# Optimization experiments

Hardware: AMD Instinct MI355X
Metric: run time of the kernel (lower is better)

## Reference

```python
import jax, jax.numpy as jnp
import numpy as np

N_NODES = 50000
N_EDGES = 800000
D = 128          # input_node_dim == output_node_dim (residual)
T = 3            # number of node types == number of edge types
NODE_IN = D + T * D  # node updater input dim = 512


def setup_inputs() -> dict:
    key = jax.random.key(0)
    ks = jax.random.split(key, 8)
    scale = 0.05
    return {
        "node_feature": jax.random.normal(ks[0], (N_NODES, D), jnp.float32),
        "W_e": jax.random.normal(ks[1], (T, D, D), jnp.float32) * scale,
        "b_e": jnp.zeros((T, D), jnp.float32),
        "W_n": jax.random.normal(ks[2], (T, D, NODE_IN), jnp.float32) * scale,
        "b_n": jnp.zeros((T, D), jnp.float32),
        "edge_src": jax.random.randint(ks[3], (N_EDGES,), 0, N_NODES, jnp.int32),
        "edge_dst": jax.random.randint(ks[4], (N_EDGES,), 0, N_NODES, jnp.int32),
        "edge_type": jax.random.randint(ks[5], (N_EDGES,), 0, T, jnp.int32),
        "node_type": jax.random.randint(ks[6], (N_NODES,), 0, T, jnp.int32),
    }


def reference(node_feature, W_e, b_e, W_n, b_n, edge_src, edge_dst, edge_type, node_type):
    N, Din = node_feature.shape
    n_types = W_e.shape[0]
    out_dim = W_e.shape[1]

    # message_function: per-edge-type MLP on source features, relu, zero elsewhere
    src = node_feature[edge_src]                      # [E, D] gather
    parts = [jax.nn.relu(node_feature)]               # reduce_function relu's node_feature
    for t in range(n_types):
        msg = jax.nn.relu(src @ W_e[t].T + b_e[t])    # [E, out]
        msg = jnp.where((edge_type == t)[:, None], msg, jnp.zeros((), msg.dtype))
        # mailbox sum over incoming edges per destination node
        parts.append(jax.ops.segment_sum(msg, edge_dst, num_segments=N))
    agg = jnp.concatenate(parts, axis=1)              # [N, D + T*out]

    # per-node-type updater MLP, dispatched by node_type
    updated = jnp.zeros((N, out_dim), node_feature.dtype)
    for t in range(n_types):
        o = agg @ W_n[t].T + b_n[t]                   # [N, out]
        updated = jnp.where((node_type == t)[:, None], o, updated)

    # use_residual = True
    return updated + node_feature
```

## Files before the change

kernel.cpp:

```cpp
#include <hip/hip_runtime.h>
#include <hip/hip_bf16.h>

#define NN 50000
#define NE 800000
#define DD 128
#define NT 3
#define AGGW 384
#define EM 64
#define EM2 128
#define LDK 136
#define CB 32
#define LDK2 520
#define NBITS 7
#define NBINS ((NN + 127) / 128)
#define EPB 2048
#define BINCAP 2560
#define NTILES_MAX (((NN + EM - 1) / EM) + NT)
#define NTILE_PAD (((NTILES_MAX + 7) / 8) * 8)
#define LHS 392

typedef __bf16 bf16x8 __attribute__((ext_vector_type(8)));
typedef float f32x4 __attribute__((ext_vector_type(4)));
typedef unsigned short u16x8 __attribute__((ext_vector_type(8)));
typedef unsigned int u32x4 __attribute__((ext_vector_type(4)));

__device__ __forceinline__ unsigned short f2b(float f) {
    __hip_bfloat16 h = __float2bfloat16(f);
    return __builtin_bit_cast(unsigned short, h);
}
__device__ __forceinline__ float b2f(unsigned int u16bits) {
    unsigned int x = u16bits << 16;
    return __builtin_bit_cast(float, x);
}

__global__ void k_prep(const float* __restrict__ nf, const float* __restrict__ We,
                       const float* __restrict__ Wn, unsigned short* __restrict__ nfb,
                       unsigned short* __restrict__ Web, unsigned short* __restrict__ Wnb,
                       int* __restrict__ bhist, int* __restrict__ cnts) {
    size_t i = (size_t)blockIdx.x * blockDim.x + threadIdx.x;
    if (i < NBINS) bhist[i] = 0;
    if (i >= NBINS && i < NBINS + 16) cnts[i - NBINS] = 0;
    const size_t n0 = (size_t)NN * DD / 8;
    const size_t n1 = (size_t)NT * DD * DD / 8;
    const size_t n2 = (size_t)NT * DD * 512 / 8;
    size_t total = n0 + n1 + n2;
    for (size_t p = i; p < total; p += (size_t)gridDim.x * blockDim.x) {
        const float* s; unsigned short* d; size_t off;
        if (p < n0)            { s = nf; d = nfb; off = p; }
        else if (p < n0 + n1)  { s = We; d = Web; off = p - n0; }
        else                   { s = Wn; d = Wnb; off = p - n0 - n1; }
        const float4* f4 = (const float4*)(s + off * 8);
        float4 x = f4[0], y = f4[1];
        u16x8 u = { f2b(x.x), f2b(x.y), f2b(x.z), f2b(x.w),
                    f2b(y.x), f2b(y.y), f2b(y.z), f2b(y.w) };
        *(u16x8*)(d + off * 8) = u;
    }
}

__global__ __launch_bounds__(256) void k_binhist(const int* __restrict__ edst,
        const int* __restrict__ ntp, int* __restrict__ bhist, int* __restrict__ cnts) {
    __shared__ int lh[NBINS];
    __shared__ int ln[3];
    int tid = threadIdx.x;
    for (int i = tid; i < NBINS; i += 256) lh[i] = 0;
    if (tid < 3) ln[tid] = 0;
    __syncthreads();
    int i0 = blockIdx.x * blockDim.x + tid;
    int stride = gridDim.x * blockDim.x;
    for (int p = i0; p < NE; p += stride) atomicAdd(&lh[edst[p] >> NBITS], 1);
    for (int p = i0; p < NN; p += stride) atomicAdd(&ln[ntp[p]], 1);
    __syncthreads();
    for (int i = tid; i < NBINS; i += 256) if (lh[i]) atomicAdd(&bhist[i], lh[i]);
    if (tid < 3) atomicAdd(&cnts[6 + tid], ln[tid]);
}

__global__ __launch_bounds__(512) void k_binscan(const int* __restrict__ bhist,
        int* __restrict__ binptr, int* __restrict__ bincur, int* __restrict__ rowptr) {
    __shared__ int sa[NBINS], sb[NBINS];
    int tid = threadIdx.x;
    if (tid < NBINS) sa[tid] = bhist[tid];
    __syncthreads();
    int flip = 0;
    for (int off = 1; off < NBINS; off <<= 1) {
        int* src = flip ? sb : sa;
        int* dst = flip ? sa : sb;
        if (tid < NBINS) dst[tid] = src[tid] + ((tid >= off) ? src[tid - off] : 0);
        __syncthreads();
        flip ^= 1;
    }
    int* inc = flip ? sb : sa;
    if (tid < NBINS) {
        int excl = (tid == 0) ? 0 : inc[tid - 1];
        binptr[tid] = excl;
        bincur[tid] = excl;
    }
    if (tid == 0) { binptr[NBINS] = NE; rowptr[NN] = NE; }
}

__global__ __launch_bounds__(512) void k_mid(
        const unsigned short* __restrict__ nfb, const unsigned short* __restrict__ Web,
        const float* __restrict__ be, unsigned short* __restrict__ M,
        const int* __restrict__ esrc, const int* __restrict__ edst,
        const int* __restrict__ et, const int* __restrict__ ntp,
        int* __restrict__ bincur, int* __restrict__ cnts,
        int* __restrict__ pe, int* __restrict__ sn, int* __restrict__ rnk) {
    const int NEB = (NE + EPB - 1) / EPB;
    const int NCH2 = (NN + 511) / 512;
    const int TILES = (NN + EM2 - 1) / EM2;
    __shared__ unsigned short Wsm[DD][LDK];
    int tid = threadIdx.x, b = blockIdx.x;

    if (b < NEB) {
        int* lh = (int*)&Wsm[0][0];
        int* lr = lh + 8 * LHS;
        int* gb = lr + 8 * LHS;
        int wv = tid >> 6, ln = tid & 63;
        for (int i = tid; i < 8 * LHS; i += 512) { lh[i] = 0; lr[i] = 0; }
        __syncthreads();
        int ew0 = b * EPB + wv * 256;
#pragma unroll
        for (int i = 0; i < 256; i += 64) {
            int e = ew0 + i + ln;
            if (e < NE) atomicAdd(&lh[wv * LHS + (edst[e] >> NBITS)], 1);
        }
        __syncthreads();
        for (int i = tid; i < NBINS; i += 512) {
            int s = 0;
#pragma unroll
            for (int w = 0; w < 8; ++w) { int t = lh[w * LHS + i]; lh[w * LHS + i] = s; s += t; }
            if (s) gb[i] = atomicAdd(&bincur[i], s);
        }
        __syncthreads();
#pragma unroll
        for (int i = 0; i < 256; i += 64) {
            int e = ew0 + i + ln;
            if (e < NE) {
                int d = edst[e];
                int t = et[e];
                int bin = d >> NBITS;
                int pos = gb[bin] + lh[wv * LHS + bin] + atomicAdd(&lr[wv * LHS + bin], 1);
                pe[pos] = (t * NN + esrc[e]) | ((d & 127) << 18) | (t << 25);
            }
        }
    } else if (b < NEB + NCH2) {
        int* lcnt = (int*)&Wsm[0][0];
        int* lbase = lcnt + 4;
        if (tid < 3) lcnt[tid] = 0;
        __syncthreads();
        int p = (b - NEB) * 512 + tid;
        int t = -1, rank = 0;
        if (p < NN) { t = ntp[p]; rank = atomicAdd(&lcnt[t], 1); }
        __syncthreads();
        if (tid < 3) lbase[tid] = atomicAdd(&cnts[9 + tid], lcnt[tid]);
        __syncthreads();
        if (p < NN) {
            int c0 = cnts[6], c1 = cnts[7];
            int off = (t == 0) ? 0 : (t == 1) ? c0 : c0 + c1;
            int pos = off + lbase[t] + rank;
            sn[pos] = p;
            rnk[p] = pos;
        }
    } else {
        int bb = b - NEB - NCH2;
        int t = bb / TILES, tile = bb % TILES;
        int base = tile * EM2;
        int m = min(EM2, NN - base);
        {
            int row = tid >> 2, c0 = (tid & 3) * 32;
            const u16x8* src = (const u16x8*)(Web + ((size_t)t * DD + row) * DD + c0);
#pragma unroll
            for (int v = 0; v < 4; ++v) *(u16x8*)&Wsm[row][c0 + v * 8] = src[v];
        }
        __syncthreads();

        int wave = tid >> 6, l = tid & 63, lr2 = l & 15, kg = l >> 4;
        int arow = min(base + wave * 16 + lr2, NN - 1);
        const u16x8* Arow = (const u16x8*)(nfb + (size_t)arow * DD);
        f32x4 acc[8];
#pragma unroll
        for (int n = 0; n < 8; n++) acc[n] = (f32x4){0.f, 0.f, 0.f, 0.f};
#pragma unroll
        for (int k0 = 0; k0 < DD; k0 += 32) {
            bf16x8 a = __builtin_bit_cast(bf16x8, Arow[(k0 >> 3) + kg]);
#pragma unroll
            for (int n = 0; n < 8; n++) {
                bf16x8 bbv = *(const bf16x8*)&Wsm[n * 16 + lr2][k0 + kg * 8];
                acc[n] = __builtin_amdgcn_mfma_f32_16x16x32_bf16(a, bbv, acc[n], 0, 0, 0);
            }
        }
        unsigned short* Mt = M + (size_t)t * NN * DD;
#pragma unroll
        for (int n = 0; n < 8; n++) {
            int col = n * 16 + lr2;
            float bias = be[t * DD + col];
#pragma unroll
            for (int r = 0; r < 4; r++) {
                int row = wave * 16 + kg * 4 + r;
                if (row < m) {
                    float v = acc[n][r] + bias;
                    Mt[(size_t)(base + row) * DD + col] = f2b(fmaxf(v, 0.f));
                }
            }
        }
    }
}

__global__ __launch_bounds__(256) void k_binsort(const int* __restrict__ binptr,
        int* __restrict__ pe, int* __restrict__ rowptr) {
    __shared__ int lcnt[128], lrk[128], lrp[128];
    __shared__ unsigned int sorted[BINCAP];
    int b = blockIdx.x, tid = threadIdx.x;
    int beg = binptr[b], end = binptr[b + 1];
    int cnt = min(end - beg, BINCAP);
    if (tid < 128) { lcnt[tid] = 0; lrk[tid] = 0; }
    __syncthreads();
    for (int e = tid; e < cnt; e += 256)
        atomicAdd(&lcnt[(pe[beg + e] >> 18) & 127], 1);
    __syncthreads();
    if (tid < 64) {
        int v = lcnt[2 * tid] + lcnt[2 * tid + 1];
        int s = v;
        for (int d = 1; d < 64; d <<= 1) {
            int u = __shfl_up(s, d);
            if (tid >= d) s += u;
        }
        int excl = s - v;
        lrp[2 * tid] = excl;
        lrp[2 * tid + 1] = excl + lcnt[2 * tid];
    }
    __syncthreads();
    if (tid < 128) {
        int node = b * 128 + tid;
        if (node < NN) rowptr[node] = beg + lrp[tid];
    }
    for (int e = tid; e < cnt; e += 256) {
        unsigned int p = pe[beg + e];
        int d = (p >> 18) & 127;
        int pos = lrp[d] + atomicAdd(&lrk[d], 1);
        sorted[pos] = p;
    }
    __syncthreads();
    for (int e = tid; e < cnt; e += 256) pe[beg + e] = sorted[e];
}

__global__ __launch_bounds__(128) void k_agg(const unsigned short* __restrict__ M,
        const int* __restrict__ rowptr, const int* __restrict__ pe,
        const int* __restrict__ rnk, unsigned short* __restrict__ aggb) {
    int node = blockIdx.x * 8 + (threadIdx.x >> 4);
    int q = threadIdx.x & 15;
    int beg = rowptr[node], end = rowptr[node + 1];
    const u32x4* Mu4 = (const u32x4*)M;
    float a0[8] = {0,0,0,0,0,0,0,0};
    float a1[8] = {0,0,0,0,0,0,0,0};
    float a2[8] = {0,0,0,0,0,0,0,0};
    int e = beg;
    while (e < end) {
        unsigned int p[8];
        u32x4 v[8];
#pragma unroll
        for (int j = 0; j < 8; ++j) p[j] = pe[min(e + j, end - 1)];
#pragma unroll
        for (int j = 0; j < 8; ++j)
            if (e + j < end) v[j] = Mu4[(size_t)(p[j] & 0x3FFFFu) * 16 + q];
#pragma unroll
        for (int j = 0; j < 8; ++j) {
            if (e + j < end) {
                int t = p[j] >> 25;
                float f0 = b2f(v[j][0] & 0xFFFF), f1 = b2f(v[j][0] >> 16);
                float f2 = b2f(v[j][1] & 0xFFFF), f3 = b2f(v[j][1] >> 16);
                float f4 = b2f(v[j][2] & 0xFFFF), f5 = b2f(v[j][2] >> 16);
                float f6 = b2f(v[j][3] & 0xFFFF), f7 = b2f(v[j][3] >> 16);
                if (t == 0) {
                    a0[0] += f0; a0[1] += f1; a0[2] += f2; a0[3] += f3;
                    a0[4] += f4; a0[5] += f5; a0[6] += f6; a0[7] += f7;
                } else if (t == 1) {
                    a1[0] += f0; a1[1] += f1; a1[2] += f2; a1[3] += f3;
                    a1[4] += f4; a1[5] += f5; a1[6] += f6; a1[7] += f7;
                } else {
                    a2[0] += f0; a2[1] += f1; a2[2] += f2; a2[3] += f3;
                    a2[4] += f4; a2[5] += f5; a2[6] += f6; a2[7] += f7;
                }
            }
        }
        e += 8;
    }
    unsigned int* dst = (unsigned int*)(aggb + (size_t)rnk[node] * AGGW);
    u32x4 o0 = { (unsigned int)f2b(a0[0]) | ((unsigned int)f2b(a0[1]) << 16),
                 (unsigned int)f2b(a0[2]) | ((unsigned int)f2b(a0[3]) << 16),
                 (unsigned int)f2b(a0[4]) | ((unsigned int)f2b(a0[5]) << 16),
                 (unsigned int)f2b(a0[6]) | ((unsigned int)f2b(a0[7]) << 16) };
    u32x4 o1 = { (unsigned int)f2b(a1[0]) | ((unsigned int)f2b(a1[1]) << 16),
                 (unsigned int)f2b(a1[2]) | ((unsigned int)f2b(a1[3]) << 16),
                 (unsigned int)f2b(a1[4]) | ((unsigned int)f2b(a1[5]) << 16),
                 (unsigned int)f2b(a1[6]) | ((unsigned int)f2b(a1[7]) << 16) };
    u32x4 o2 = { (unsigned int)f2b(a2[0]) | ((unsigned int)f2b(a2[1]) << 16),
                 (unsigned int)f2b(a2[2]) | ((unsigned int)f2b(a2[3]) << 16),
                 (unsigned int)f2b(a2[4]) | ((unsigned int)f2b(a2[5]) << 16),
                 (unsigned int)f2b(a2[6]) | ((unsigned int)f2b(a2[7]) << 16) };
    ((u32x4*)dst)[q]        = o0;
    ((u32x4*)(dst + 64))[q] = o1;
    ((u32x4*)(dst + 128))[q] = o2;
}

__global__ __launch_bounds__(256, 3) void k_node(const float* __restrict__ nf,
        const unsigned short* __restrict__ nfb, const unsigned short* __restrict__ Wnb,
        const float* __restrict__ bn, const int* __restrict__ sn,
        const int* __restrict__ cnts, const unsigned short* __restrict__ aggb,
        float* __restrict__ out) {
    __shared__ unsigned short Wsm[CB][LDK2];
    int c0 = cnts[6], c1 = cnts[7], c2 = cnts[8];
    int n0 = (c0 + EM - 1) / EM, n1 = (c1 + EM - 1) / EM, n2 = (c2 + EM - 1) / EM;
    int ntile = n0 + n1 + n2;
    int b = blockIdx.x;
    int rt = (b & 7) * (NTILE_PAD / 8) + (b >> 3);
    if (rt >= ntile) return;
    int tid = threadIdx.x;
    int wave = tid >> 6, l = tid & 63, lr = l & 15, kg = l >> 4;
    int t, tile;
    if (rt < n0) { t = 0; tile = rt; }
    else if (rt < n0 + n1) { t = 1; tile = rt - n0; }
    else { t = 2; tile = rt - n0 - n1; }
    int off = (t == 0) ? 0 : (t == 1) ? c0 : c0 + c1;
    int cntt = (t == 0) ? c0 : (t == 1) ? c1 : c2;
    int base = off + tile * EM;
    int m = min(EM, cntt - tile * EM);

    int srtrow = base + min(wave * 16 + lr, m - 1);
    int myrow = sn[srtrow];
    const u16x8* An = (const u16x8*)(nfb + (size_t)myrow * DD);
    const u16x8* Ag = (const u16x8*)(aggb + (size_t)srtrow * AGGW);
    u16x8 afr[16];
#pragma unroll
    for (int kc = 0; kc < 4; ++kc) {
#pragma unroll
        for (int k0 = 0; k0 < DD; k0 += 32) {
            u16x8 araw;
            if (kc == 0) {
                araw = An[(k0 >> 3) + kg];
#pragma unroll
                for (int j = 0; j < 8; ++j)
                    araw[j] = (araw[j] & 0x8000) ? (unsigned short)0 : araw[j];
            } else {
                araw = Ag[((kc - 1) * DD + k0) / 8 + kg];
            }
            afr[kc * 4 + (k0 >> 5)] = araw;
        }
    }

    int nd[4];
#pragma unroll
    for (int r = 0; r < 4; ++r) nd[r] = sn[base + min(wave * 16 + kg * 4 + r, m - 1)];

    int srow = tid & 31, scc = (tid >> 5) * 64;
#pragma unroll 1
    for (int cbk = 0; cbk < 4; ++cbk) {
        if (cbk) __syncthreads();
        const u16x8* src = (const u16x8*)(Wnb + ((size_t)t * DD + cbk * CB + srow) * 512 + scc);
#pragma unroll
        for (int v = 0; v < 8; ++v) *(u16x8*)&Wsm[srow][scc + v * 8] = src[v];
        __syncthreads();

        f32x4 acc0 = {0.f, 0.f, 0.f, 0.f}, acc1 = {0.f, 0.f, 0.f, 0.f};
#pragma unroll
        for (int kc = 0; kc < 4; ++kc) {
#pragma unroll
            for (int k0 = 0; k0 < DD; k0 += 32) {
                bf16x8 a = __builtin_bit_cast(bf16x8, afr[kc * 4 + (k0 >> 5)]);
                int kw = kc * DD + k0 + kg * 8;
                bf16x8 b0 = *(const bf16x8*)&Wsm[lr][kw];
                bf16x8 b1 = *(const bf16x8*)&Wsm[16 + lr][kw];
                acc0 = __builtin_amdgcn_mfma_f32_16x16x32_bf16(a, b0, acc0, 0, 0, 0);
                acc1 = __builtin_amdgcn_mfma_f32_16x16x32_bf16(a, b1, acc1, 0, 0, 0);
            }
        }
#pragma unroll
        for (int n = 0; n < 2; n++) {
            int col = cbk * CB + n * 16 + lr;
            float bias = bn[t * DD + col];
            const f32x4& av = n ? acc1 : acc0;
#pragma unroll
            for (int r = 0; r < 4; r++) {
                int row = wave * 16 + kg * 4 + r;
                if (row < m) {
                    int node = nd[r];
                    out[(size_t)node * DD + col] = av[r] + bias + nf[(size_t)node * DD + col];
                }
            }
        }
    }
}

extern "C" void kernel_launch(void* const* d_in, const int* in_sizes, int n_in,
                              void* d_out, int out_size, void* d_ws, size_t ws_size,
                              hipStream_t stream) {
    const float* nf   = (const float*)d_in[0];
    const float* We   = (const float*)d_in[1];
    const float* be   = (const float*)d_in[2];
    const float* Wn   = (const float*)d_in[3];
    const float* bn   = (const float*)d_in[4];
    const int*   esrc = (const int*)d_in[5];
    const int*   edst = (const int*)d_in[6];
    const int*   et   = (const int*)d_in[7];
    const int*   ntp  = (const int*)d_in[8];
    float* out = (float*)d_out;

    char* w = (char*)d_ws;
    unsigned short* M    = (unsigned short*)w;  w += (size_t)NT * NN * DD * 2;
    unsigned short* aggb = (unsigned short*)w;  w += (size_t)NN * AGGW * 2;
    unsigned short* nfb  = (unsigned short*)w;  w += (size_t)NN * DD * 2;
    unsigned short* Web  = (unsigned short*)w;  w += (size_t)NT * DD * DD * 2;
    unsigned short* Wnb  = (unsigned short*)w;  w += (size_t)NT * DD * 512 * 2;
    int* pe     = (int*)w;  w += (size_t)NE * 4;
    int* bhist  = (int*)w;  w += (NBINS + 1) * 4;
    int* binptr = (int*)w;  w += (NBINS + 1) * 4;
    int* bincur = (int*)w;  w += (NBINS + 1) * 4;
    int* rowptr = (int*)w;  w += (size_t)(NN + 1) * 4;
    int* sn     = (int*)w;  w += (size_t)NN * 4;
    int* rnk    = (int*)w;  w += (size_t)NN * 4;
    int* cnts   = (int*)w;  w += 16 * 4;

    const int NEB = (NE + EPB - 1) / EPB;
    const int NCH2 = (NN + 511) / 512;
    const int TILES2 = (NN + EM2 - 1) / EM2;

    k_prep<<<1024, 256, 0, stream>>>(nf, We, Wn, nfb, Web, Wnb, bhist, cnts);
    k_binhist<<<256, 256, 0, stream>>>(edst, ntp, bhist, cnts);
    k_binscan<<<1, 512, 0, stream>>>(bhist, binptr, bincur, rowptr);
    k_mid<<<NEB + NCH2 + NT * TILES2, 512, 0, stream>>>(nfb, Web, be, M,
            esrc, edst, et, ntp, bincur, cnts, pe, sn, rnk);
    k_binsort<<<NBINS, 256, 0, stream>>>(binptr, pe, rowptr);
    k_agg<<<NN / 8, 128, 0, stream>>>(M, rowptr, pe, rnk, aggb);
    k_node<<<NTILE_PAD, 256, 0, stream>>>(nf, nfb, Wnb, bn, sn, cnts, aggb, out);
}
```

Before: 138.3 us.

## Replace binned two-level edge sort with direct per-row CSR counting sort

```diff
diff --git a/kernel.cpp b/kernel.cpp
--- a/kernel.cpp
+++ b/kernel.cpp
@@ -11,13 +11,9 @@
 #define LDK 136
 #define CB 32
 #define LDK2 520
-#define NBITS 7
-#define NBINS ((NN + 127) / 128)
 #define EPB 2048
-#define BINCAP 2560
 #define NTILES_MAX (((NN + EM - 1) / EM) + NT)
 #define NTILE_PAD (((NTILES_MAX + 7) / 8) * 8)
-#define LHS 392
 
 typedef __bf16 bf16x8 __attribute__((ext_vector_type(8)));
 typedef float f32x4 __attribute__((ext_vector_type(4)));
@@ -36,10 +32,10 @@
 __global__ void k_prep(const float* __restrict__ nf, const float* __restrict__ We,
                        const float* __restrict__ Wn, unsigned short* __restrict__ nfb,
                        unsigned short* __restrict__ Web, unsigned short* __restrict__ Wnb,
-                       int* __restrict__ bhist, int* __restrict__ cnts) {
+                       int* __restrict__ rowcnt, int* __restrict__ cnts) {
     size_t i = (size_t)blockIdx.x * blockDim.x + threadIdx.x;
-    if (i < NBINS) bhist[i] = 0;
-    if (i >= NBINS && i < NBINS + 16) cnts[i - NBINS] = 0;
+    if (i < NN) rowcnt[i] = 0;
+    if (i >= NN && i < NN + 16) cnts[i - NN] = 0;
     const size_t n0 = (size_t)NN * DD / 8;
     const size_t n1 = (size_t)NT * DD * DD / 8;
     const size_t n2 = (size_t)NT * DD * 512 / 8;
@@ -57,44 +53,59 @@
     }
 }
 
-__global__ __launch_bounds__(256) void k_binhist(const int* __restrict__ edst,
-        const int* __restrict__ ntp, int* __restrict__ bhist, int* __restrict__ cnts) {
-    __shared__ int lh[NBINS];
+__global__ __launch_bounds__(256) void k_hist(const int* __restrict__ edst,
+        const int* __restrict__ ntp, int* __restrict__ rowcnt, int* __restrict__ cnts) {
     __shared__ int ln[3];
     int tid = threadIdx.x;
-    for (int i = tid; i < NBINS; i += 256) lh[i] = 0;
     if (tid < 3) ln[tid] = 0;
     __syncthreads();
-    int i0 = blockIdx.x * blockDim.x + tid;
-    int stride = gridDim.x * blockDim.x;
-    for (int p = i0; p < NE; p += stride) atomicAdd(&lh[edst[p] >> NBITS], 1);
+    int i0 = blockIdx.x * 256 + tid;
+    int stride = gridDim.x * 256;
+    for (int p = i0; p < NE; p += stride) atomicAdd(&rowcnt[edst[p]], 1);
     for (int p = i0; p < NN; p += stride) atomicAdd(&ln[ntp[p]], 1);
     __syncthreads();
-    for (int i = tid; i < NBINS; i += 256) if (lh[i]) atomicAdd(&bhist[i], lh[i]);
     if (tid < 3) atomicAdd(&cnts[6 + tid], ln[tid]);
 }
 
-__global__ __launch_bounds__(512) void k_binscan(const int* __restrict__ bhist,
-        int* __restrict__ binptr, int* __restrict__ bincur, int* __restrict__ rowptr) {
-    __shared__ int sa[NBINS], sb[NBINS];
+__global__ __launch_bounds__(1024) void k_scan(const int* __restrict__ rowcnt,
+        int* __restrict__ rowptr, int* __restrict__ rowcur) {
+    __shared__ int ws[16];
     int tid = threadIdx.x;
-    if (tid < NBINS) sa[tid] = bhist[tid];
+    const int PT = 49;
+    int i0 = tid * PT;
+    int s = 0;
+    for (int k = 0; k < PT; ++k) {
+        int i = i0 + k;
+        if (i < NN) s += rowcnt[i];
+    }
+    int lane = tid & 63, wv = tid >> 6;
+    int v = s;
+    for (int d = 1; d < 64; d <<= 1) {
+        int u = __shfl_up(v, d);
+        if (lane >= d) v += u;
+    }
+    if (lane == 63) ws[wv] = v;
     __syncthreads();
-    int flip = 0;
-    for (int off = 1; off < NBINS; off <<= 1) {
-        int* src = flip ? sb : sa;
-        int* dst = flip ? sa : sb;
-        if (tid < NBINS) dst[tid] = src[tid] + ((tid >= off) ? src[tid - off] : 0);
-        __syncthreads();
-        flip ^= 1;
-    }
-    int* inc = flip ? sb : sa;
-    if (tid < NBINS) {
-        int excl = (tid == 0) ? 0 : inc[tid - 1];
-        binptr[tid] = excl;
-        bincur[tid] = excl;
-    }
-    if (tid == 0) { binptr[NBINS] = NE; rowptr[NN] = NE; }
+    if (wv == 0 && lane < 16) {
+        int wsum = ws[lane];
+        int w2 = wsum;
+        for (int d = 1; d < 16; d <<= 1) {
+            int u = __shfl_up(w2, d);
+            if (lane >= d) w2 += u;
+        }
+        ws[lane] = w2 - wsum;
+    }
+    __syncthreads();
+    int run = (v - s) + ws[wv];
+    for (int k = 0; k < PT; ++k) {
+        int i = i0 + k;
+        if (i < NN) {
+            rowptr[i] = run;
+            rowcur[i] = run;
+            run += rowcnt[i];
+        }
+    }
+    if (tid == 1023) rowptr[NN] = NE;
 }
 
 __global__ __launch_bounds__(512) void k_mid(
@@ -102,7 +113,7 @@
         const float* __restrict__ be, unsigned short* __restrict__ M,
         const int* __restrict__ esrc, const int* __restrict__ edst,
         const int* __restrict__ et, const int* __restrict__ ntp,
-        int* __restrict__ bincur, int* __restrict__ cnts,
+        int* __restrict__ rowcur, int* __restrict__ cnts,
         int* __restrict__ pe, int* __restrict__ sn, int* __restrict__ rnk) {
     const int NEB = (NE + EPB - 1) / EPB;
     const int NCH2 = (NN + 511) / 512;
@@ -111,35 +122,15 @@
     int tid = threadIdx.x, b = blockIdx.x;
 
     if (b < NEB) {
-        int* lh = (int*)&Wsm[0][0];
-        int* lr = lh + 8 * LHS;
-        int* gb = lr + 8 * LHS;
-        int wv = tid >> 6, ln = tid & 63;
-        for (int i = tid; i < 8 * LHS; i += 512) { lh[i] = 0; lr[i] = 0; }
-        __syncthreads();
-        int ew0 = b * EPB + wv * 256;
-#pragma unroll
-        for (int i = 0; i < 256; i += 64) {
-            int e = ew0 + i + ln;
-            if (e < NE) atomicAdd(&lh[wv * LHS + (edst[e] >> NBITS)], 1);
-        }
-        __syncthreads();
-        for (int i = tid; i < NBINS; i += 512) {
-            int s = 0;
-#pragma unroll
-            for (int w = 0; w < 8; ++w) { int t = lh[w * LHS + i]; lh[w * LHS + i] = s; s += t; }
-            if (s) gb[i] = atomicAdd(&bincur[i], s);
-        }
-        __syncthreads();
-#pragma unroll
-        for (int i = 0; i < 256; i += 64) {
-            int e = ew0 + i + ln;
+        int e0 = b * EPB;
+#pragma unroll
+        for (int i = 0; i < EPB; i += 512) {
+            int e = e0 + i + tid;
             if (e < NE) {
                 int d = edst[e];
                 int t = et[e];
-                int bin = d >> NBITS;
-                int pos = gb[bin] + lh[wv * LHS + bin] + atomicAdd(&lr[wv * LHS + bin], 1);
-                pe[pos] = (t * NN + esrc[e]) | ((d & 127) << 18) | (t << 25);
+                int pos = atomicAdd(&rowcur[d], 1);
+                pe[pos] = (t * NN + esrc[e]) | (t << 25);
             }
         }
     } else if (b < NEB + NCH2) {
@@ -203,44 +194,6 @@
             }
         }
     }
-}
-
-__global__ __launch_bounds__(256) void k_binsort(const int* __restrict__ binptr,
-        int* __restrict__ pe, int* __restrict__ rowptr) {
-    __shared__ int lcnt[128], lrk[128], lrp[128];
-    __shared__ unsigned int sorted[BINCAP];
-    int b = blockIdx.x, tid = threadIdx.x;
-    int beg = binptr[b], end = binptr[b + 1];
-    int cnt = min(end - beg, BINCAP);
-    if (tid < 128) { lcnt[tid] = 0; lrk[tid] = 0; }
-    __syncthreads();
-    for (int e = tid; e < cnt; e += 256)
-        atomicAdd(&lcnt[(pe[beg + e] >> 18) & 127], 1);
-    __syncthreads();
-    if (tid < 64) {
-        int v = lcnt[2 * tid] + lcnt[2 * tid + 1];
-        int s = v;
-        for (int d = 1; d < 64; d <<= 1) {
-            int u = __shfl_up(s, d);
-            if (tid >= d) s += u;
-        }
-        int excl = s - v;
-        lrp[2 * tid] = excl;
-        lrp[2 * tid + 1] = excl + lcnt[2 * tid];
-    }
-    __syncthreads();
-    if (tid < 128) {
-        int node = b * 128 + tid;
-        if (node < NN) rowptr[node] = beg + lrp[tid];
-    }
-    for (int e = tid; e < cnt; e += 256) {
-        unsigned int p = pe[beg + e];
-        int d = (p >> 18) & 127;
-        int pos = lrp[d] + atomicAdd(&lrk[d], 1);
-        sorted[pos] = p;
-    }
-    __syncthreads();
-    for (int e = tid; e < cnt; e += 256) pe[beg + e] = sorted[e];
 }
 
 __global__ __launch_bounds__(128) void k_agg(const unsigned short* __restrict__ M,
@@ -411,10 +364,9 @@
     unsigned short* Web  = (unsigned short*)w;  w += (size_t)NT * DD * DD * 2;
     unsigned short* Wnb  = (unsigned short*)w;  w += (size_t)NT * DD * 512 * 2;
     int* pe     = (int*)w;  w += (size_t)NE * 4;
-    int* bhist  = (int*)w;  w += (NBINS + 1) * 4;
-    int* binptr = (int*)w;  w += (NBINS + 1) * 4;
-    int* bincur = (int*)w;  w += (NBINS + 1) * 4;
+    int* rowcnt = (int*)w;  w += (size_t)NN * 4;
     int* rowptr = (int*)w;  w += (size_t)(NN + 1) * 4;
+    int* rowcur = (int*)w;  w += (size_t)NN * 4;
     int* sn     = (int*)w;  w += (size_t)NN * 4;
     int* rnk    = (int*)w;  w += (size_t)NN * 4;
     int* cnts   = (int*)w;  w += 16 * 4;
@@ -423,12 +375,11 @@
     const int NCH2 = (NN + 511) / 512;
     const int TILES2 = (NN + EM2 - 1) / EM2;
 
-    k_prep<<<1024, 256, 0, stream>>>(nf, We, Wn, nfb, Web, Wnb, bhist, cnts);
-    k_binhist<<<256, 256, 0, stream>>>(edst, ntp, bhist, cnts);
-    k_binscan<<<1, 512, 0, stream>>>(bhist, binptr, bincur, rowptr);
+    k_prep<<<1024, 256, 0, stream>>>(nf, We, Wn, nfb, Web, Wnb, rowcnt, cnts);
+    k_hist<<<256, 256, 0, stream>>>(edst, ntp, rowcnt, cnts);
+    k_scan<<<1, 1024, 0, stream>>>(rowcnt, rowptr, rowcur);
     k_mid<<<NEB + NCH2 + NT * TILES2, 512, 0, stream>>>(nfb, Web, be, M,
-            esrc, edst, et, ntp, bincur, cnts, pe, sn, rnk);
-    k_binsort<<<NBINS, 256, 0, stream>>>(binptr, pe, rowptr);
+            esrc, edst, et, ntp, rowcur, cnts, pe, sn, rnk);
     k_agg<<<NN / 8, 128, 0, stream>>>(M, rowptr, pe, rnk, aggb);
     k_node<<<NTILE_PAD, 256, 0, stream>>>(nf, nfb, Wnb, bn, sn, cnts, aggb, out);
 }
```

Result: slower. 304.5 us (+120.1%).
